# Performance work log

Measured on AMD Instinct MI355X. Metric: run time of the kernel, lower is better.

## Reference

```python
import jax, jax.numpy as jnp
import numpy as np

FEATURE_DIM = 512
SQRT_DIM = float(np.sqrt(FEATURE_DIM))


def setup_inputs() -> dict:
    key = jax.random.key(0)
    x = jax.random.normal(key, (5, FEATURE_DIM, 128, 256), dtype=jnp.float32)
    return {"x": x, "record_len": 4}


def reference(x, record_len):
    # x: [max_cav, C, H, W]; record_len: python int (number of valid CAVs)
    max_cav, C, H, W = x.shape
    # tokens: [H*W, max_cav, C]
    tokens = x.reshape(max_cav, C, H * W).transpose(2, 0, 1)
    # scores: [H*W, max_cav, max_cav]
    score = jnp.einsum('bqc,bkc->bqk', tokens, tokens) / SQRT_DIM
    # pad mask over key dim: keys with index >= record_len are invalid
    pad_mask = jnp.arange(max_cav) >= record_len            # [max_cav]
    score = jnp.where(pad_mask[None, None, :], -jnp.inf, score)
    attn = jax.nn.softmax(score, axis=-1)
    attn = jnp.nan_to_num(attn, nan=0.0)                    # all-masked rows -> 0
    context = jnp.einsum('bqk,bkc->bqc', attn, tokens)      # [H*W, max_cav, C]
    ego = context[:, 0, :]                                  # [H*W, C]
    return ego.T.reshape(C, H, W)[None]                     # [1, C, H, W]
```

## Files before the change

### kernel.cpp

```cpp
#include <hip/hip_runtime.h>
#include <math.h>

#define KMAX   5
#define NC     512
#define HW     32768
#define NCHUNK 8
#define CPC    (NC / NCHUNK)
#define INV_SQRT_DIM 0.044194173824159216f

__device__ __forceinline__ int clamp_K(const int* __restrict__ rlp) {
    int K = *rlp;
    return K < 0 ? 0 : (K > KMAX ? KMAX : K);
}

__global__ void k1_partial_dots(const float* __restrict__ x,
                                const int* __restrict__ rlp,
                                float* __restrict__ partial) {
    const int b4    = blockIdx.x * blockDim.x + threadIdx.x;
    const int chunk = blockIdx.y;
    const int K     = clamp_K(rlp);
    const float4* xv = (const float4*)x;

    float4 d[KMAX];
#pragma unroll
    for (int k = 0; k < KMAX; ++k) d[k] = make_float4(0.f, 0.f, 0.f, 0.f);

    const int c0 = chunk * CPC;
#pragma unroll 4
    for (int c = c0; c < c0 + CPC; ++c) {
        const float4 x0 = xv[(size_t)c * (HW / 4) + b4];
        d[0].x += x0.x * x0.x; d[0].y += x0.y * x0.y;
        d[0].z += x0.z * x0.z; d[0].w += x0.w * x0.w;
#pragma unroll
        for (int k = 1; k < KMAX; ++k) {
            if (k < K) {
                const float4 xk = xv[((size_t)k * NC + c) * (HW / 4) + b4];
                d[k].x += x0.x * xk.x; d[k].y += x0.y * xk.y;
                d[k].z += x0.z * xk.z; d[k].w += x0.w * xk.w;
            }
        }
    }

    float4* pv = (float4*)partial;
#pragma unroll
    for (int k = 0; k < KMAX; ++k)
        if (k < K) pv[((size_t)chunk * KMAX + k) * (HW / 4) + b4] = d[k];
}

__global__ void k2_softmax(const float* __restrict__ partial,
                           const int* __restrict__ rlp,
                           float* __restrict__ attn) {
    const int b = blockIdx.x * blockDim.x + threadIdx.x;
    const int K = clamp_K(rlp);

    float d[KMAX];
#pragma unroll
    for (int k = 0; k < KMAX; ++k) d[k] = 0.f;
    for (int ch = 0; ch < NCHUNK; ++ch) {
#pragma unroll
        for (int k = 0; k < KMAX; ++k)
            if (k < K) d[k] += partial[((size_t)ch * KMAX + k) * HW + b];
    }

    float m = -INFINITY;
#pragma unroll
    for (int k = 0; k < KMAX; ++k)
        if (k < K) { d[k] *= INV_SQRT_DIM; if (d[k] > m) m = d[k]; }
    float s = 0.f;
#pragma unroll
    for (int k = 0; k < KMAX; ++k)
        if (k < K) { d[k] = expf(d[k] - m); s += d[k]; }
    const float inv = (K > 0) ? 1.f / s : 0.f;
#pragma unroll
    for (int k = 0; k < KMAX; ++k)
        attn[(size_t)k * HW + b] = (k < K) ? d[k] * inv : 0.f;
}

__global__ void k1_full_softmax(const float* __restrict__ x,
                                const int* __restrict__ rlp,
                                float* __restrict__ attn) {
    const int b4 = blockIdx.x * blockDim.x + threadIdx.x;
    const int K  = clamp_K(rlp);
    const float4* xv = (const float4*)x;

    float4 d[KMAX];
#pragma unroll
    for (int k = 0; k < KMAX; ++k) d[k] = make_float4(0.f, 0.f, 0.f, 0.f);

#pragma unroll 4
    for (int c = 0; c < NC; ++c) {
        const float4 x0 = xv[(size_t)c * (HW / 4) + b4];
        d[0].x += x0.x * x0.x; d[0].y += x0.y * x0.y;
        d[0].z += x0.z * x0.z; d[0].w += x0.w * x0.w;
#pragma unroll
        for (int k = 1; k < KMAX; ++k) {
            if (k < K) {
                const float4 xk = xv[((size_t)k * NC + c) * (HW / 4) + b4];
                d[k].x += x0.x * xk.x; d[k].y += x0.y * xk.y;
                d[k].z += x0.z * xk.z; d[k].w += x0.w * xk.w;
            }
        }
    }

    float4 m = make_float4(-INFINITY, -INFINITY, -INFINITY, -INFINITY);
#pragma unroll
    for (int k = 0; k < KMAX; ++k)
        if (k < K) {
            d[k].x *= INV_SQRT_DIM; d[k].y *= INV_SQRT_DIM;
            d[k].z *= INV_SQRT_DIM; d[k].w *= INV_SQRT_DIM;
            m.x = fmaxf(m.x, d[k].x); m.y = fmaxf(m.y, d[k].y);
            m.z = fmaxf(m.z, d[k].z); m.w = fmaxf(m.w, d[k].w);
        }
    float4 s = make_float4(0.f, 0.f, 0.f, 0.f);
#pragma unroll
    for (int k = 0; k < KMAX; ++k)
        if (k < K) {
            d[k].x = expf(d[k].x - m.x); d[k].y = expf(d[k].y - m.y);
            d[k].z = expf(d[k].z - m.z); d[k].w = expf(d[k].w - m.w);
            s.x += d[k].x; s.y += d[k].y; s.z += d[k].z; s.w += d[k].w;
        }
    float4 inv = make_float4(0.f, 0.f, 0.f, 0.f);
    if (K > 0) { inv.x = 1.f / s.x; inv.y = 1.f / s.y; inv.z = 1.f / s.z; inv.w = 1.f / s.w; }

    float4* av = (float4*)attn;
#pragma unroll
    for (int k = 0; k < KMAX; ++k) {
        float4 a = make_float4(0.f, 0.f, 0.f, 0.f);
        if (k < K) {
            a.x = d[k].x * inv.x; a.y = d[k].y * inv.y;
            a.z = d[k].z * inv.z; a.w = d[k].w * inv.w;
        }
        av[(size_t)k * (HW / 4) + b4] = a;
    }
}

__global__ void k3_out(const float* __restrict__ x,
                       const int* __restrict__ rlp,
                       const float* __restrict__ attn,
                       float* __restrict__ out) {
    const int idx = blockIdx.x * blockDim.x + threadIdx.x;
    const int b4  = idx & (HW / 4 - 1);
    const int c   = idx >> 13;
    const int K   = clamp_K(rlp);

    const float4* xv = (const float4*)x;
    const float4* av = (const float4*)attn;

    float4 acc = make_float4(0.f, 0.f, 0.f, 0.f);
#pragma unroll
    for (int k = 0; k < KMAX; ++k) {
        if (k < K) {
            const float4 a  = av[(size_t)k * (HW / 4) + b4];
            const float4 xk = xv[((size_t)k * NC + c) * (HW / 4) + b4];
            acc.x += a.x * xk.x; acc.y += a.y * xk.y;
            acc.z += a.z * xk.z; acc.w += a.w * xk.w;
        }
    }
    ((float4*)out)[(size_t)c * (HW / 4) + b4] = acc;
}

extern "C" void kernel_launch(void* const* d_in, const int* in_sizes, int n_in,
                              void* d_out, int out_size, void* d_ws, size_t ws_size,
                              hipStream_t stream) {
    const float* x  = (const float*)d_in[0];
    const int*   rl = (const int*)d_in[1];
    float*       out = (float*)d_out;
    float*       ws  = (float*)d_ws;

    const size_t partial_elems = (size_t)NCHUNK * KMAX * HW;
    const size_t attn_elems    = (size_t)KMAX * HW;

    if (ws_size >= (partial_elems + attn_elems) * sizeof(float)) {
        float* partial = ws;
        float* attn    = ws + partial_elems;
        k1_partial_dots<<<dim3((HW / 4) / 256, NCHUNK), 256, 0, stream>>>(x, rl, partial);
        k2_softmax<<<HW / 256, 256, 0, stream>>>(partial, rl, attn);
        k3_out<<<(NC * (HW / 4)) / 256, 256, 0, stream>>>(x, rl, attn, out);
    } else {
        float* attn = ws;
        k1_full_softmax<<<(HW / 4) / 256, 256, 0, stream>>>(x, rl, attn);
        k3_out<<<(NC * (HW / 4)) / 256, 256, 0, stream>>>(x, rl, attn, out);
    }
}
```

Before: 537.3 us.

## Specialize kernels on record_len via templates and split channel reduction into more chunks

Each kernel now dispatches on the runtime K value to a template instantiation, so the inner loops unroll fully with no per-k branch. Channel chunks for the partial dot products go from 8 to 32, giving 4x more blocks in the first kernel to raise occupancy and memory-level parallelism. The cost is a larger partial buffer that the softmax kernel must read and reduce, a larger workspace requirement that may send small workspaces to the fallback path, and more code size.

```diff
diff --git a/kernel.cpp b/kernel.cpp
--- a/kernel.cpp
+++ b/kernel.cpp
@@ -4,13 +4,40 @@
 #define KMAX   5
 #define NC     512
 #define HW     32768
-#define NCHUNK 8
+#define NCHUNK 32
 #define CPC    (NC / NCHUNK)
 #define INV_SQRT_DIM 0.044194173824159216f
 
 __device__ __forceinline__ int clamp_K(const int* __restrict__ rlp) {
     int K = *rlp;
     return K < 0 ? 0 : (K > KMAX ? KMAX : K);
+}
+
+template <int K>
+__device__ __forceinline__ void k1_dots_body(const float4* __restrict__ xv,
+                                             float4* __restrict__ pv,
+                                             int b4, int chunk) {
+    float4 d[K];
+#pragma unroll
+    for (int k = 0; k < K; ++k) d[k] = make_float4(0.f, 0.f, 0.f, 0.f);
+
+    const int c0 = chunk * CPC;
+#pragma unroll 4
+    for (int i = 0; i < CPC; ++i) {
+        const int c = c0 + i;
+        const float4 x0 = xv[(size_t)c * (HW / 4) + b4];
+        d[0].x += x0.x * x0.x; d[0].y += x0.y * x0.y;
+        d[0].z += x0.z * x0.z; d[0].w += x0.w * x0.w;
+#pragma unroll
+        for (int k = 1; k < K; ++k) {
+            const float4 xk = xv[((size_t)k * NC + c) * (HW / 4) + b4];
+            d[k].x += x0.x * xk.x; d[k].y += x0.y * xk.y;
+            d[k].z += x0.z * xk.z; d[k].w += x0.w * xk.w;
+        }
+    }
+#pragma unroll
+    for (int k = 0; k < K; ++k)
+        pv[((size_t)chunk * KMAX + k) * (HW / 4) + b4] = d[k];
 }
 
 __global__ void k1_partial_dots(const float* __restrict__ x,
@@ -20,31 +47,39 @@
     const int chunk = blockIdx.y;
     const int K     = clamp_K(rlp);
     const float4* xv = (const float4*)x;
-
-    float4 d[KMAX];
-#pragma unroll
-    for (int k = 0; k < KMAX; ++k) d[k] = make_float4(0.f, 0.f, 0.f, 0.f);
-
-    const int c0 = chunk * CPC;
+    float4*       pv = (float4*)partial;
+    switch (K) {
+        case 1: k1_dots_body<1>(xv, pv, b4, chunk); break;
+        case 2: k1_dots_body<2>(xv, pv, b4, chunk); break;
+        case 3: k1_dots_body<3>(xv, pv, b4, chunk); break;
+        case 4: k1_dots_body<4>(xv, pv, b4, chunk); break;
+        case 5: k1_dots_body<5>(xv, pv, b4, chunk); break;
+        default: break;
+    }
+}
+
+template <int K>
+__device__ __forceinline__ void k2_body(const float* __restrict__ partial,
+                                        float* __restrict__ attn, int b) {
+    float d[K];
+#pragma unroll
+    for (int k = 0; k < K; ++k) d[k] = 0.f;
 #pragma unroll 4
-    for (int c = c0; c < c0 + CPC; ++c) {
-        const float4 x0 = xv[(size_t)c * (HW / 4) + b4];
-        d[0].x += x0.x * x0.x; d[0].y += x0.y * x0.y;
-        d[0].z += x0.z * x0.z; d[0].w += x0.w * x0.w;
-#pragma unroll
-        for (int k = 1; k < KMAX; ++k) {
-            if (k < K) {
-                const float4 xk = xv[((size_t)k * NC + c) * (HW / 4) + b4];
-                d[k].x += x0.x * xk.x; d[k].y += x0.y * xk.y;
-                d[k].z += x0.z * xk.z; d[k].w += x0.w * xk.w;
-            }
-        }
-    }
-
-    float4* pv = (float4*)partial;
+    for (int ch = 0; ch < NCHUNK; ++ch) {
+#pragma unroll
+        for (int k = 0; k < K; ++k)
+            d[k] += partial[((size_t)ch * KMAX + k) * HW + b];
+    }
+    float m = -INFINITY;
+#pragma unroll
+    for (int k = 0; k < K; ++k) { d[k] *= INV_SQRT_DIM; m = fmaxf(m, d[k]); }
+    float s = 0.f;
+#pragma unroll
+    for (int k = 0; k < K; ++k) { d[k] = expf(d[k] - m); s += d[k]; }
+    const float inv = 1.f / s;
 #pragma unroll
     for (int k = 0; k < KMAX; ++k)
-        if (k < K) pv[((size_t)chunk * KMAX + k) * (HW / 4) + b4] = d[k];
+        attn[(size_t)k * HW + b] = (k < K) ? d[k] * inv : 0.f;
 }
 
 __global__ void k2_softmax(const float* __restrict__ partial,
@@ -52,86 +87,33 @@
                            float* __restrict__ attn) {
     const int b = blockIdx.x * blockDim.x + threadIdx.x;
     const int K = clamp_K(rlp);
-
-    float d[KMAX];
-#pragma unroll
-    for (int k = 0; k < KMAX; ++k) d[k] = 0.f;
-    for (int ch = 0; ch < NCHUNK; ++ch) {
-#pragma unroll
-        for (int k = 0; k < KMAX; ++k)
-            if (k < K) d[k] += partial[((size_t)ch * KMAX + k) * HW + b];
-    }
-
-    float m = -INFINITY;
-#pragma unroll
-    for (int k = 0; k < KMAX; ++k)
-        if (k < K) { d[k] *= INV_SQRT_DIM; if (d[k] > m) m = d[k]; }
-    float s = 0.f;
-#pragma unroll
-    for (int k = 0; k < KMAX; ++k)
-        if (k < K) { d[k] = expf(d[k] - m); s += d[k]; }
-    const float inv = (K > 0) ? 1.f / s : 0.f;
-#pragma unroll
-    for (int k = 0; k < KMAX; ++k)
-        attn[(size_t)k * HW + b] = (k < K) ? d[k] * inv : 0.f;
-}
-
-__global__ void k1_full_softmax(const float* __restrict__ x,
-                                const int* __restrict__ rlp,
-                                float* __restrict__ attn) {
-    const int b4 = blockIdx.x * blockDim.x + threadIdx.x;
-    const int K  = clamp_K(rlp);
-    const float4* xv = (const float4*)x;
-
-    float4 d[KMAX];
-#pragma unroll
-    for (int k = 0; k < KMAX; ++k) d[k] = make_float4(0.f, 0.f, 0.f, 0.f);
-
-#pragma unroll 4
-    for (int c = 0; c < NC; ++c) {
-        const float4 x0 = xv[(size_t)c * (HW / 4) + b4];
-        d[0].x += x0.x * x0.x; d[0].y += x0.y * x0.y;
-        d[0].z += x0.z * x0.z; d[0].w += x0.w * x0.w;
-#pragma unroll
-        for (int k = 1; k < KMAX; ++k) {
-            if (k < K) {
-                const float4 xk = xv[((size_t)k * NC + c) * (HW / 4) + b4];
-                d[k].x += x0.x * xk.x; d[k].y += x0.y * xk.y;
-                d[k].z += x0.z * xk.z; d[k].w += x0.w * xk.w;
-            }
-        }
-    }
-
-    float4 m = make_float4(-INFINITY, -INFINITY, -INFINITY, -INFINITY);
-#pragma unroll
-    for (int k = 0; k < KMAX; ++k)
-        if (k < K) {
-            d[k].x *= INV_SQRT_DIM; d[k].y *= INV_SQRT_DIM;
-            d[k].z *= INV_SQRT_DIM; d[k].w *= INV_SQRT_DIM;
-            m.x = fmaxf(m.x, d[k].x); m.y = fmaxf(m.y, d[k].y);
-            m.z = fmaxf(m.z, d[k].z); m.w = fmaxf(m.w, d[k].w);
-        }
-    float4 s = make_float4(0.f, 0.f, 0.f, 0.f);
-#pragma unroll
-    for (int k = 0; k < KMAX; ++k)
-        if (k < K) {
-            d[k].x = expf(d[k].x - m.x); d[k].y = expf(d[k].y - m.y);
-            d[k].z = expf(d[k].z - m.z); d[k].w = expf(d[k].w - m.w);
-            s.x += d[k].x; s.y += d[k].y; s.z += d[k].z; s.w += d[k].w;
-        }
-    float4 inv = make_float4(0.f, 0.f, 0.f, 0.f);
-    if (K > 0) { inv.x = 1.f / s.x; inv.y = 1.f / s.y; inv.z = 1.f / s.z; inv.w = 1.f / s.w; }
-
-    float4* av = (float4*)attn;
-#pragma unroll
-    for (int k = 0; k < KMAX; ++k) {
-        float4 a = make_float4(0.f, 0.f, 0.f, 0.f);
-        if (k < K) {
-            a.x = d[k].x * inv.x; a.y = d[k].y * inv.y;
-            a.z = d[k].z * inv.z; a.w = d[k].w * inv.w;
-        }
-        av[(size_t)k * (HW / 4) + b4] = a;
-    }
+    switch (K) {
+        case 1: k2_body<1>(partial, attn, b); break;
+        case 2: k2_body<2>(partial, attn, b); break;
+        case 3: k2_body<3>(partial, attn, b); break;
+        case 4: k2_body<4>(partial, attn, b); break;
+        case 5: k2_body<5>(partial, attn, b); break;
+        default:
+#pragma unroll
+            for (int k = 0; k < KMAX; ++k) attn[(size_t)k * HW + b] = 0.f;
+            break;
+    }
+}
+
+template <int K>
+__device__ __forceinline__ void k3_body(const float4* __restrict__ xv,
+                                        const float4* __restrict__ av,
+                                        float4* __restrict__ outv,
+                                        int b4, int c) {
+    float4 acc = make_float4(0.f, 0.f, 0.f, 0.f);
+#pragma unroll
+    for (int k = 0; k < K; ++k) {
+        const float4 a  = av[(size_t)k * (HW / 4) + b4];
+        const float4 xk = xv[((size_t)k * NC + c) * (HW / 4) + b4];
+        acc.x += a.x * xk.x; acc.y += a.y * xk.y;
+        acc.z += a.z * xk.z; acc.w += a.w * xk.w;
+    }
+    outv[(size_t)c * (HW / 4) + b4] = acc;
 }
 
 __global__ void k3_out(const float* __restrict__ x,
@@ -142,28 +124,84 @@
     const int b4  = idx & (HW / 4 - 1);
     const int c   = idx >> 13;
     const int K   = clamp_K(rlp);
-
+    const float4* xv   = (const float4*)x;
+    const float4* av   = (const float4*)attn;
+    float4*       outv = (float4*)out;
+    switch (K) {
+        case 1: k3_body<1>(xv, av, outv, b4, c); break;
+        case 2: k3_body<2>(xv, av, outv, b4, c); break;
+        case 3: k3_body<3>(xv, av, outv, b4, c); break;
+        case 4: k3_body<4>(xv, av, outv, b4, c); break;
+        case 5: k3_body<5>(xv, av, outv, b4, c); break;
+        default:
+            outv[(size_t)c * (HW / 4) + b4] = make_float4(0.f, 0.f, 0.f, 0.f);
+            break;
+    }
+}
+
+__global__ void k1_full_softmax(const float* __restrict__ x,
+                                const int* __restrict__ rlp,
+                                float* __restrict__ attn) {
+    const int b4 = blockIdx.x * blockDim.x + threadIdx.x;
+    const int K  = clamp_K(rlp);
     const float4* xv = (const float4*)x;
-    const float4* av = (const float4*)attn;
-
-    float4 acc = make_float4(0.f, 0.f, 0.f, 0.f);
+
+    float4 d[KMAX];
+#pragma unroll
+    for (int k = 0; k < KMAX; ++k) d[k] = make_float4(0.f, 0.f, 0.f, 0.f);
+
+#pragma unroll 4
+    for (int c = 0; c < NC; ++c) {
+        const float4 x0 = xv[(size_t)c * (HW / 4) + b4];
+        d[0].x += x0.x * x0.x; d[0].y += x0.y * x0.y;
+        d[0].z += x0.z * x0.z; d[0].w += x0.w * x0.w;
+#pragma unroll
+        for (int k = 1; k < KMAX; ++k) {
+            if (k < K) {
+                const float4 xk = xv[((size_t)k * NC + c) * (HW / 4) + b4];
+                d[k].x += x0.x * xk.x; d[k].y += x0.y * xk.y;
+                d[k].z += x0.z * xk.z; d[k].w += x0.w * xk.w;
+            }
+        }
+    }
+
+    float4 m = make_float4(-INFINITY, -INFINITY, -INFINITY, -INFINITY);
+#pragma unroll
+    for (int k = 0; k < KMAX; ++k)
+        if (k < K) {
+            d[k].x *= INV_SQRT_DIM; d[k].y *= INV_SQRT_DIM;
+            d[k].z *= INV_SQRT_DIM; d[k].w *= INV_SQRT_DIM;
+            m.x = fmaxf(m.x, d[k].x); m.y = fmaxf(m.y, d[k].y);
+            m.z = fmaxf(m.z, d[k].z); m.w = fmaxf(m.w, d[k].w);
+        }
+    float4 s = make_float4(0.f, 0.f, 0.f, 0.f);
+#pragma unroll
+    for (int k = 0; k < KMAX; ++k)
+        if (k < K) {
+            d[k].x = expf(d[k].x - m.x); d[k].y = expf(d[k].y - m.y);
+            d[k].z = expf(d[k].z - m.z); d[k].w = expf(d[k].w - m.w);
+            s.x += d[k].x; s.y += d[k].y; s.z += d[k].z; s.w += d[k].w;
+        }
+    float4 inv = make_float4(0.f, 0.f, 0.f, 0.f);
+    if (K > 0) { inv.x = 1.f / s.x; inv.y = 1.f / s.y; inv.z = 1.f / s.z; inv.w = 1.f / s.w; }
+
+    float4* av = (float4*)attn;
 #pragma unroll
     for (int k = 0; k < KMAX; ++k) {
+        float4 a = make_float4(0.f, 0.f, 0.f, 0.f);
         if (k < K) {
-            const float4 a  = av[(size_t)k * (HW / 4) + b4];
-            const float4 xk = xv[((size_t)k * NC + c) * (HW / 4) + b4];
-            acc.x += a.x * xk.x; acc.y += a.y * xk.y;
-            acc.z += a.z * xk.z; acc.w += a.w * xk.w;
-        }
-    }
-    ((float4*)out)[(size_t)c * (HW / 4) + b4] = acc;
+            a.x = d[k].x * inv.x; a.y = d[k].y * inv.y;
+            a.z = d[k].z * inv.z; a.w = d[k].w * inv.w;
+        }
+        av[(size_t)k * (HW / 4) + b4] = a;
+    }
 }
 
 extern "C" void kernel_launch(void* const* d_in, const int* in_sizes, int n_in,
                               void* d_out, int out_size, void* d_ws, size_t ws_size,
                               hipStream_t stream) {
-    const float* x  = (const float*)d_in[0];
-    const int*   rl = (const int*)d_in[1];
+    const float* x   = (const float*)d_in[0];
+    const int*   rl  = (const int*)d_in[1];
     float*       out = (float*)d_out;
     float*       ws  = (float*)d_ws;
 
```

Result: faster. 493.8 us (-8.1%).
